# Kernel optimization log

Hardware: AMD Instinct MI355X
Metric: run time of the kernel (lower is better)

The kernel has to match this reference:

```python
import jax, jax.numpy as jnp
import numpy as np

S = 2048  # expert group size
M = 768   # hidden size
H = 3072  # intermediate size
E = 16    # num experts


def top2_gating(gates):
    # gates: [G, S, E]
    G, S_, E_ = gates.shape
    C = 2 * S_ // E_
    mask_dtype = jnp.int32
    index_1 = jnp.argmax(gates, axis=-1)
    mask_1 = jax.nn.one_hot(index_1, E_, dtype=mask_dtype)
    gate_1 = jnp.einsum('GSE,GSE->GS', gates, mask_1)
    gates_without_top_1 = gates * (1 - mask_1)
    index_2 = jnp.argmax(gates_without_top_1, axis=-1)
    mask_2 = jax.nn.one_hot(index_2, E_, dtype=mask_dtype)
    gate_2 = jnp.einsum('GSE,GSE->GS', gates_without_top_1, mask_2)
    pos_1 = jnp.cumsum(mask_1, axis=-2) - mask_1
    mask_1 = mask_1 * (pos_1 < C)
    pos_1 = jnp.einsum('GSE,GSE->GS', pos_1, mask_1)
    mask_1_count = jnp.sum(mask_1, axis=-2)
    mask_1_flat = jnp.sum(mask_1, axis=-1)
    pos_2 = jnp.cumsum(mask_2, axis=-2) - mask_2 + jnp.expand_dims(mask_1_count, -2)
    mask_2 = mask_2 * (pos_2 < C)
    pos_2 = jnp.einsum('GSE,GSE->GS', pos_2, mask_2)
    mask_2_flat = jnp.sum(mask_2, axis=-1)
    gate_1 = gate_1 * mask_1_flat
    gate_2 = gate_2 * mask_2_flat
    denom = gate_1 + gate_2
    denom = jnp.where(denom > 0, denom, jnp.ones_like(denom))
    gate_1 = gate_1 / denom
    gate_2 = gate_2 / denom
    a = jnp.expand_dims(gate_1 * mask_1_flat, -1) * jax.nn.one_hot(index_1, E_, dtype=gates.dtype)
    b = jax.nn.one_hot(pos_1, C, dtype=gates.dtype)
    first = jnp.einsum('GSE,GSC->GSEC', a, b)
    a = jnp.expand_dims(gate_2 * mask_2_flat, -1) * jax.nn.one_hot(index_2, E_, dtype=gates.dtype)
    b = jax.nn.one_hot(pos_2, C, dtype=gates.dtype)
    second = jnp.einsum('GSE,GSC->GSEC', a, b)
    combined_tensor = first + second
    dispatch_tensor = combined_tensor.astype(jnp.bool_)
    return combined_tensor, dispatch_tensor


def setup_inputs() -> dict:
    key = jax.random.key(0)
    k1, k2, k3, k4 = jax.random.split(key, 4)
    inputs = jax.random.normal(k1, (4, 1024, M), dtype=jnp.float32)
    wg = jax.random.normal(k2, (M, E), dtype=jnp.float32) * (1.0 / np.sqrt(M))
    wi = jax.random.normal(k3, (E, M, H), dtype=jnp.float32) * (1.0 / np.sqrt(M))
    wo = jax.random.normal(k4, (E, H, M), dtype=jnp.float32) * (1.0 / np.sqrt(H))
    return {"inputs": inputs, "wg": wg, "wi": wi, "wo": wo}


def reference(inputs, wg, wi, wo):
    x = jnp.reshape(inputs, (-1, S, M))                      # [G, S, M]
    gates = jax.nn.softmax(jnp.einsum('GSM,ME->GSE', x, wg))
    combined_weights, dispatch_mask = top2_gating(gates)
    dispatched = jnp.einsum('GSEC,GSM->EGCM',
                            dispatch_mask.astype(x.dtype), x)
    h = jnp.einsum('EGCM,EMH->EGCH', dispatched, wi)
    h = jax.nn.relu(h)
    expert_out = jnp.einsum('EGCH,EHM->GECM', h, wo)
    out = jnp.einsum('GSEC,GECM->GSM', combined_weights, expert_out)
    return jnp.reshape(out, inputs.shape)
```

## Files before the change

### kernel.cpp

```cpp
#include <hip/hip_runtime.h>
#include <hip/hip_bf16.h>
#include <cstdint>
#include <cstddef>

#define S_TOK 2048
#define M_DIM 768
#define H_DIM 3072
#define E_NUM 16
#define CAP   256

using s16x8 = __attribute__((ext_vector_type(8))) short;
using f32x4 = __attribute__((ext_vector_type(4))) float;

__device__ __forceinline__ unsigned short f2bf(float f) {
    unsigned u = __float_as_uint(f);
    unsigned r = 0x7fffu + ((u >> 16) & 1u);
    return (unsigned short)((u + r) >> 16);
}

__device__ __forceinline__ void async16(const void* g, void* l) {
    __builtin_amdgcn_global_load_lds((const __attribute__((address_space(1))) void*)g,
                                     (__attribute__((address_space(3))) void*)l, 16, 0, 0);
}

__global__ void gating_kernel(const float* __restrict__ x, const float* __restrict__ wg,
                              int* __restrict__ e1o, int* __restrict__ e2o,
                              float* __restrict__ g1o, float* __restrict__ g2o, int ntok) {
    int gid  = blockIdx.x * blockDim.x + threadIdx.x;
    int tok  = gid >> 6;
    int lane = threadIdx.x & 63;
    if (tok >= ntok) return;
    const float* xr = x + (size_t)tok * M_DIM;
    float acc[E_NUM];
#pragma unroll
    for (int e = 0; e < E_NUM; ++e) acc[e] = 0.f;
    for (int m = lane; m < M_DIM; m += 64) {
        float xv = xr[m];
        const float* wr = wg + (size_t)m * E_NUM;
#pragma unroll
        for (int e = 0; e < E_NUM; ++e) acc[e] += xv * wr[e];
    }
#pragma unroll
    for (int off = 32; off >= 1; off >>= 1) {
#pragma unroll
        for (int e = 0; e < E_NUM; ++e) acc[e] += __shfl_xor(acc[e], off, 64);
    }
    if (lane == 0) {
        float mx = acc[0];
#pragma unroll
        for (int e = 1; e < E_NUM; ++e) mx = fmaxf(mx, acc[e]);
        float p[E_NUM]; float s = 0.f;
#pragma unroll
        for (int e = 0; e < E_NUM; ++e) { p[e] = expf(acc[e] - mx); s += p[e]; }
        float inv = 1.f / s;
        int b1 = 0; float v1 = -1.f;
#pragma unroll
        for (int e = 0; e < E_NUM; ++e) { if (p[e] > v1) { v1 = p[e]; b1 = e; } }
        int b2 = 0; float v2 = -1.f;
#pragma unroll
        for (int e = 0; e < E_NUM; ++e) { if (e != b1 && p[e] > v2) { v2 = p[e]; b2 = e; } }
        e1o[tok] = b1; e2o[tok] = b2;
        g1o[tok] = v1 * inv; g2o[tok] = v2 * inv;
    }
}

__global__ void assign_kernel(const int* __restrict__ e1a, const int* __restrict__ e2a,
                              const float* __restrict__ g1a, const float* __restrict__ g2a,
                              int* __restrict__ slot1, int* __restrict__ slot2,
                              float* __restrict__ w1, float* __restrict__ w2,
                              int* __restrict__ tfs, int G) {
    int g    = blockIdx.x;
    int tid  = threadIdx.x;
    int w    = tid >> 6;
    int lane = tid & 63;
    __shared__ int cnt1s[E_NUM];

    for (int i = tid; i < E_NUM * CAP; i += 1024) tfs[(size_t)g * E_NUM * CAP + i] = -1;
    __syncthreads();

    {
        int cnt = 0;
        for (int base = 0; base < S_TOK; base += 64) {
            int t = g * S_TOK + base + lane;
            bool pred = (e1a[t] == w);
            unsigned long long bal = __ballot(pred);
            int prefix = __popcll(bal & ((1ull << lane) - 1ull));
            if (pred) {
                int pos = cnt + prefix;
                if (pos < CAP) {
                    slot1[t] = w * CAP + pos;
                    tfs[((size_t)g * E_NUM + w) * CAP + pos] = base + lane;
                } else {
                    slot1[t] = -1;
                }
            }
            cnt += __popcll(bal);
        }
        if (lane == 0) cnt1s[w] = cnt < CAP ? cnt : CAP;
    }
    __syncthreads();
    {
        int cnt = cnt1s[w];
        for (int base = 0; base < S_TOK; base += 64) {
            int t = g * S_TOK + base + lane;
            bool pred = (e2a[t] == w);
            unsigned long long bal = __ballot(pred);
            int prefix = __popcll(bal & ((1ull << lane) - 1ull));
            if (pred) {
                int pos = cnt + prefix;
                if (pos < CAP) {
                    slot2[t] = w * CAP + pos;
                    tfs[((size_t)g * E_NUM + w) * CAP + pos] = base + lane;
                } else {
                    slot2[t] = -1;
                }
            }
            cnt += __popcll(bal);
        }
    }
    __syncthreads();
    for (int t = tid; t < S_TOK; t += 1024) {
        int gt = g * S_TOK + t;
        float a = slot1[gt] >= 0 ? g1a[gt] : 0.f;
        float b = slot2[gt] >= 0 ? g2a[gt] : 0.f;
        float denom = a + b;
        if (!(denom > 0.f)) denom = 1.f;
        w1[gt] = a / denom;
        w2[gt] = b / denom;
    }
}

__global__ void convert_x_kernel(const float* __restrict__ x, unsigned short* __restrict__ xb,
                                 int ntok) {
    int i4 = blockIdx.x * blockDim.x + threadIdx.x;
    size_t base = (size_t)i4 * 4;
    size_t n_real = (size_t)ntok * M_DIM;
    size_t n_tot  = (size_t)(ntok + 1) * M_DIM;
    if (base >= n_tot) return;
    ushort4 o;
    if (base < n_real) {
        float4 v = *(const float4*)&x[base];
        o.x = f2bf(v.x); o.y = f2bf(v.y); o.z = f2bf(v.z); o.w = f2bf(v.w);
    } else {
        o.x = o.y = o.z = o.w = 0;
    }
    *(ushort4*)&xb[base] = o;
}

__global__ __launch_bounds__(256) void transpose_conv_kernel(const float* __restrict__ src,
                                                             unsigned short* __restrict__ dst,
                                                             int R, int C) {
    __shared__ float T[64][65];
    int e  = blockIdx.z;
    int c0 = blockIdx.x * 64;
    int r0 = blockIdx.y * 64;
    int tid = threadIdx.x;
    int lx = tid & 63, ly = tid >> 6;
    const float* S = src + (size_t)e * R * C;
#pragma unroll
    for (int i = 0; i < 16; ++i) {
        int r = i * 4 + ly;
        T[r][lx] = S[(size_t)(r0 + r) * C + c0 + lx];
    }
    __syncthreads();
    unsigned short* D = dst + (size_t)e * C * R;
#pragma unroll
    for (int i = 0; i < 16; ++i) {
        int c = i * 4 + ly;
        D[(size_t)(c0 + c) * R + r0 + lx] = f2bf(T[lx][c]);
    }
}

template<int KLEN, bool GATHER>
__global__ __launch_bounds__(256) void mfma_gemm_kernel(
        const unsigned short* __restrict__ A,
        const unsigned short* __restrict__ B,
        const int* __restrict__ tfs,
        void* __restrict__ Out, int G, int N_total) {
    __shared__ unsigned short As[128 * 32];
    __shared__ unsigned short Bs[128 * 32];
    __shared__ int rowtok[128];

    int z  = blockIdx.z;
    int e  = z / G, g = z % G;
    int n0 = blockIdx.x * 128;
    int c0 = blockIdx.y * 128;
    int tid = threadIdx.x;

    if (GATHER) {
        if (tid < 128) rowtok[tid] = tfs[((size_t)g * E_NUM + e) * CAP + c0 + tid];
        __syncthreads();
    }

    int r4 = tid >> 2, l4 = tid & 3;
    const unsigned short *apt0, *apt1;
    if (GATHER) {
        int t0 = rowtok[r4], t1 = rowtok[64 + r4];
        size_t row0 = (t0 < 0) ? (size_t)(G * S_TOK) : (size_t)(g * S_TOK + t0);
        size_t row1 = (t1 < 0) ? (size_t)(G * S_TOK) : (size_t)(g * S_TOK + t1);
        apt0 = A + row0 * KLEN + l4 * 8;
        apt1 = A + row1 * KLEN + l4 * 8;
    } else {
        apt0 = A + ((size_t)z * CAP + c0 + r4) * KLEN + l4 * 8;
        apt1 = apt0 + (size_t)64 * KLEN;
    }
    const unsigned short* Bexp = B + (size_t)e * N_total * KLEN;
    const unsigned short* bpt0 = Bexp + ((size_t)n0 + r4) * KLEN + l4 * 8;
    const unsigned short* bpt1 = bpt0 + (size_t)64 * KLEN;

    int wv = tid >> 6;
    unsigned short* as0 = &As[(wv * 16) * 32];
    unsigned short* as1 = &As[(64 + wv * 16) * 32];
    unsigned short* bs0 = &Bs[(wv * 16) * 32];
    unsigned short* bs1 = &Bs[(64 + wv * 16) * 32];

    int lane = tid & 63;
    int r = lane & 15, q = lane >> 4;
    int wm = wv & 1, wn = wv >> 1;

    f32x4 acc[4][4];
#pragma unroll
    for (int i = 0; i < 4; ++i)
#pragma unroll
        for (int j = 0; j < 4; ++j) acc[i][j] = (f32x4)(0.f);

    for (int k0 = 0; k0 < KLEN; k0 += 32) {
        async16(apt0, as0);
        async16(apt1, as1);
        async16(bpt0, bs0);
        async16(bpt1, bs1);
        apt0 += 32; apt1 += 32; bpt0 += 32; bpt1 += 32;
        __syncthreads();
        s16x8 af[4], bfr[4];
#pragma unroll
        for (int i = 0; i < 4; ++i)
            af[i] = *(const s16x8*)&As[(wm * 64 + i * 16 + r) * 32 + q * 8];
#pragma unroll
        for (int j = 0; j < 4; ++j)
            bfr[j] = *(const s16x8*)&Bs[(wn * 64 + j * 16 + r) * 32 + q * 8];
#pragma unroll
        for (int i = 0; i < 4; ++i)
#pragma unroll
            for (int j = 0; j < 4; ++j)
                acc[i][j] = __builtin_amdgcn_mfma_f32_16x16x32_bf16(af[i], bfr[j], acc[i][j], 0, 0, 0);
        __syncthreads();
    }

    if (GATHER) {
        unsigned short* H = (unsigned short*)Out;
#pragma unroll
        for (int i = 0; i < 4; ++i) {
#pragma unroll
            for (int v = 0; v < 4; ++v) {
                int m_loc = wm * 64 + i * 16 + q * 4 + v;
                unsigned short* row = H + ((size_t)z * CAP + c0 + m_loc) * N_total + n0;
#pragma unroll
                for (int j = 0; j < 4; ++j) {
                    int n_loc = wn * 64 + j * 16 + r;
                    row[n_loc] = f2bf(fmaxf(acc[i][j][v], 0.f));
                }
            }
        }
    } else {
        float* O = (float*)Out;
#pragma unroll
        for (int i = 0; i < 4; ++i) {
#pragma unroll
            for (int v = 0; v < 4; ++v) {
                int m_loc = wm * 64 + i * 16 + q * 4 + v;
                float* row = O + (((size_t)g * E_NUM + e) * CAP + c0 + m_loc) * N_total + n0;
#pragma unroll
                for (int j = 0; j < 4; ++j) {
                    int n_loc = wn * 64 + j * 16 + r;
                    row[n_loc] = acc[i][j][v];
                }
            }
        }
    }
}

__global__ void combine_kernel(const float* __restrict__ eo,
                               const int* __restrict__ slot1, const int* __restrict__ slot2,
                               const float* __restrict__ w1, const float* __restrict__ w2,
                               float* __restrict__ out, int G) {
    int t = blockIdx.x;
    int g = t / S_TOK;
    int tid = threadIdx.x;
    int s1 = slot1[t], s2 = slot2[t];
    float a = w1[t], b = w2[t];
    const float* base_g = eo + (size_t)g * E_NUM * CAP * M_DIM;
    const float* p1 = base_g + (size_t)(s1 < 0 ? 0 : s1) * M_DIM;
    const float* p2 = base_g + (size_t)(s2 < 0 ? 0 : s2) * M_DIM;
    for (int m = tid; m < M_DIM; m += 256) {
        float v = 0.f;
        if (s1 >= 0) v += a * p1[m];
        if (s2 >= 0) v += b * p2[m];
        out[(size_t)t * M_DIM + m] = v;
    }
}

extern "C" void kernel_launch(void* const* d_in, const int* in_sizes, int n_in,
                              void* d_out, int out_size, void* d_ws, size_t ws_size,
                              hipStream_t stream) {
    const float* x  = (const float*)d_in[0];
    const float* wg = (const float*)d_in[1];
    const float* wi = (const float*)d_in[2];
    const float* wo = (const float*)d_in[3];
    float* out = (float*)d_out;

    int ntok = in_sizes[0] / M_DIM;
    int G = ntok / S_TOK;

    char* wsp = (char*)d_ws;
    auto carve = [&](size_t bytes) {
        void* p = (void*)wsp;
        wsp += (bytes + 255) & ~(size_t)255;
        return p;
    };
    int*   e1    = (int*)carve((size_t)ntok * 4);
    int*   e2    = (int*)carve((size_t)ntok * 4);
    float* g1    = (float*)carve((size_t)ntok * 4);
    float* g2    = (float*)carve((size_t)ntok * 4);
    int*   slot1 = (int*)carve((size_t)ntok * 4);
    int*   slot2 = (int*)carve((size_t)ntok * 4);
    float* w1    = (float*)carve((size_t)ntok * 4);
    float* w2    = (float*)carve((size_t)ntok * 4);
    int*   tfs   = (int*)carve((size_t)G * E_NUM * CAP * 4);
    unsigned short* xb  = (unsigned short*)carve((size_t)(ntok + 1) * M_DIM * 2);
    unsigned short* wiT = (unsigned short*)carve((size_t)E_NUM * H_DIM * M_DIM * 2);
    unsigned short* woT = (unsigned short*)carve((size_t)E_NUM * M_DIM * H_DIM * 2);
    unsigned short* h   = (unsigned short*)carve((size_t)E_NUM * G * CAP * H_DIM * 2);
    float* eo = (float*)carve((size_t)G * E_NUM * CAP * M_DIM * 4);

    gating_kernel<<<(ntok * 64 + 255) / 256, 256, 0, stream>>>(x, wg, e1, e2, g1, g2, ntok);
    assign_kernel<<<G, 1024, 0, stream>>>(e1, e2, g1, g2, slot1, slot2, w1, w2, tfs, G);

    int nx4 = ((ntok + 1) * M_DIM) / 4;
    convert_x_kernel<<<(nx4 + 255) / 256, 256, 0, stream>>>(x, xb, ntok);
    transpose_conv_kernel<<<dim3(H_DIM / 64, M_DIM / 64, E_NUM), 256, 0, stream>>>(wi, wiT, M_DIM, H_DIM);
    transpose_conv_kernel<<<dim3(M_DIM / 64, H_DIM / 64, E_NUM), 256, 0, stream>>>(wo, woT, H_DIM, M_DIM);

    mfma_gemm_kernel<M_DIM, true><<<dim3(H_DIM / 128, CAP / 128, E_NUM * G), 256, 0, stream>>>(
        xb, wiT, tfs, h, G, H_DIM);
    mfma_gemm_kernel<H_DIM, false><<<dim3(M_DIM / 128, CAP / 128, E_NUM * G), 256, 0, stream>>>(
        h, woT, tfs, eo, G, M_DIM);

    combine_kernel<<<ntok, 256, 0, stream>>>(eo, slot1, slot2, w1, w2, out, G);
}
```

Baseline: 550.6 us.

## Remap GEMM grid to 1D with XCD-aware swizzle; vectorize transpose stores

New measurement: 547.0 us. Within noise of the previous version (-0.6%).

```diff
diff --git a/kernel.cpp b/kernel.cpp
--- a/kernel.cpp
+++ b/kernel.cpp
@@ -156,18 +156,25 @@
     int r0 = blockIdx.y * 64;
     int tid = threadIdx.x;
     int lx = tid & 63, ly = tid >> 6;
-    const float* S = src + (size_t)e * R * C;
+    const float* Sp = src + (size_t)e * R * C;
 #pragma unroll
     for (int i = 0; i < 16; ++i) {
         int r = i * 4 + ly;
-        T[r][lx] = S[(size_t)(r0 + r) * C + c0 + lx];
+        T[r][lx] = Sp[(size_t)(r0 + r) * C + c0 + lx];
     }
     __syncthreads();
     unsigned short* D = dst + (size_t)e * C * R;
-#pragma unroll
-    for (int i = 0; i < 16; ++i) {
-        int c = i * 4 + ly;
-        D[(size_t)(c0 + c) * R + r0 + lx] = f2bf(T[lx][c]);
+    int rb = (tid & 15) * 4;
+    int cy = tid >> 4;
+#pragma unroll
+    for (int p = 0; p < 4; ++p) {
+        int c = p * 16 + cy;
+        ushort4 o;
+        o.x = f2bf(T[rb + 0][c]);
+        o.y = f2bf(T[rb + 1][c]);
+        o.z = f2bf(T[rb + 2][c]);
+        o.w = f2bf(T[rb + 3][c]);
+        *(ushort4*)&D[(size_t)(c0 + c) * R + r0 + rb] = o;
     }
 }
 
@@ -181,10 +188,23 @@
     __shared__ unsigned short Bs[128 * 32];
     __shared__ int rowtok[128];
 
-    int z  = blockIdx.z;
-    int e  = z / G, g = z % G;
-    int n0 = blockIdx.x * 128;
-    int c0 = blockIdx.y * 128;
+    int NB  = gridDim.x;
+    int bid = blockIdx.x;
+    int lid = bid;
+    if ((NB & 7) == 0) {
+        int per = NB >> 3;
+        lid = (bid & 7) * per + (bid >> 3);
+    }
+    int NT_N = N_total >> 7;
+    int c  = lid & 1;
+    int r1 = lid >> 1;
+    int g  = r1 % G;
+    int r2 = r1 / G;
+    int n  = r2 % NT_N;
+    int e  = r2 / NT_N;
+    int z  = e * G + g;
+    int n0 = n * 128;
+    int c0 = c * 128;
     int tid = threadIdx.x;
 
     if (GATHER) {
@@ -340,9 +360,9 @@
     transpose_conv_kernel<<<dim3(H_DIM / 64, M_DIM / 64, E_NUM), 256, 0, stream>>>(wi, wiT, M_DIM, H_DIM);
     transpose_conv_kernel<<<dim3(M_DIM / 64, H_DIM / 64, E_NUM), 256, 0, stream>>>(wo, woT, H_DIM, M_DIM);
 
-    mfma_gemm_kernel<M_DIM, true><<<dim3(H_DIM / 128, CAP / 128, E_NUM * G), 256, 0, stream>>>(
+    mfma_gemm_kernel<M_DIM, true><<<(H_DIM / 128) * (CAP / 128) * E_NUM * G, 256, 0, stream>>>(
         xb, wiT, tfs, h, G, H_DIM);
-    mfma_gemm_kernel<H_DIM, false><<<dim3(M_DIM / 128, CAP / 128, E_NUM * G), 256, 0, stream>>>(
+    mfma_gemm_kernel<H_DIM, false><<<(M_DIM / 128) * (CAP / 128) * E_NUM * G, 256, 0, stream>>>(
         h, woT, tfs, eo, G, M_DIM);
 
     combine_kernel<<<ntok, 256, 0, stream>>>(eo, slot1, slot2, w1, w2, out, G);
```
